# Performance work log

Hardware: AMD Instinct MI355X
Metric: run time of the kernel (lower is better)

## Reference

```python
import jax, jax.numpy as jnp
import numpy as np

TOP_K = 2
SCALE = 1.0  # score_scale_factor

def setup_inputs() -> dict:
    key = jax.random.key(0)
    ks = jax.random.split(key, 8)
    T, D, E, F = 4096, 1024, 8, 4096
    return {
        "hidden_states": jax.random.normal(ks[0], (T, D), jnp.float32),
        "gw1": jax.random.normal(ks[1], (D, D // 4), jnp.float32) * 0.02,
        "gb1": jnp.zeros((D // 4,), jnp.float32),
        "gw2": jax.random.normal(ks[2], (D // 4, D // 16), jnp.float32) * 0.02,
        "gb2": jnp.zeros((D // 16,), jnp.float32),
        "gw3": jax.random.normal(ks[3], (D // 16, E), jnp.float32) * 0.02,
        "w1": jax.random.normal(ks[4], (E, D, F), jnp.float32) * 0.02,
        "b1": jnp.zeros((E, F), jnp.float32),
        "w2": jax.random.normal(ks[5], (E, F, D), jnp.float32) * 0.02,
        "b2": jnp.zeros((E, D), jnp.float32),
    }

def reference(hidden_states, gw1, gb1, gw2, gb2, gw3, w1, b1, w2, b2):
    h = hidden_states                              # [T, D]
    g = jax.nn.relu(h @ gw1 + gb1)
    g = jax.nn.relu(g @ gw2 + gb2)
    router_logits = g @ gw3                        # [T, E]
    probs = jax.nn.softmax(router_logits.astype(jnp.float32), axis=-1)
    top_w, top_i = jax.lax.top_k(probs, TOP_K)     # [T, k]
    top_w = top_w / jnp.sum(top_w, axis=-1, keepdims=True)
    top_w = top_w.astype(h.dtype)
    T, E = router_logits.shape
    # combine weights: scatter normalized top-k weights into dense [T, E]
    cw = jnp.zeros((T, E), h.dtype).at[jnp.arange(T)[:, None], top_i].add(top_w)
    out = jnp.zeros_like(h)
    for e in range(E):  # small fixed expert count
        y = jax.nn.gelu(h @ w1[e] + b1[e]) @ w2[e] + b2[e]
        out = out + y * (cw[:, e:e + 1] * SCALE)
    return out, router_logits
```

## Files before the change

### kernel.cpp

```cpp
#include <hip/hip_runtime.h>
#include <stdint.h>

#define T_  4096
#define D_  1024
#define E_  8
#define F_  4096
#define H1_ 256
#define H2_ 64
#define SCALE_ 1.0f
#define NROW_ (2 * T_)
#define NTILES_ 72

typedef unsigned short ushort_t;
typedef unsigned int   uint32;
typedef __attribute__((ext_vector_type(8))) short  short8;
typedef __attribute__((ext_vector_type(4))) float  f32x4;
typedef __attribute__((ext_vector_type(8))) unsigned short us8;

#define BARRIER() do { asm volatile("" ::: "memory"); __builtin_amdgcn_s_barrier(); asm volatile("" ::: "memory"); } while (0)
#define WAITVM(N) asm volatile("s_waitcnt vmcnt(" #N ")" ::: "memory")

__device__ __forceinline__ ushort_t f2bf(float f) {
  uint32 u = __float_as_uint(f);
  u += 0x7FFFu + ((u >> 16) & 1u);
  return (ushort_t)(u >> 16);
}
__device__ __forceinline__ float gelu_tanh(float x) {
  float u = 0.7978845608028654f * (x + 0.044715f * x * x * x);
  float e = __expf(2.0f * u);
  return 0.5f * x * (1.0f + (1.0f - 2.0f / (e + 1.0f)));
}
__device__ __forceinline__ void gll16(const void* gptr, void* lptr) {
  void* g = const_cast<void*>(gptr);
  __builtin_amdgcn_global_load_lds((__attribute__((address_space(1))) void*)g,
                                   (__attribute__((address_space(3))) void*)lptr,
                                   16, 0, 0);
}

__device__ __forceinline__ void stage4(const ushort_t* a0, const ushort_t* a1,
                                       const ushort_t* b0, const ushort_t* b1,
                                       short8* An, short8* Bn, int w) {
  gll16(a0, An + (w * 2 + 0) * 64);
  gll16(a1, An + (w * 2 + 1) * 64);
  gll16(b0, Bn + (w * 2 + 0) * 64);
  gll16(b1, Bn + (w * 2 + 1) * 64);
}

__device__ __forceinline__ void mfma_step(const short8* Ac, const short8* Bc,
                                          int wr, int wc, int lane, f32x4 acc[4][4]) {
  short8 af[4], bf4[4];
#pragma unroll
  for (int i = 0; i < 4; ++i) af[i] = Ac[(wr * 4 + i) * 64 + lane];
#pragma unroll
  for (int j = 0; j < 4; ++j) bf4[j] = Bc[(wc * 4 + j) * 64 + lane];
#pragma unroll
  for (int i = 0; i < 4; ++i)
#pragma unroll
    for (int j = 0; j < 4; ++j)
      acc[i][j] = __builtin_amdgcn_mfma_f32_16x16x32_bf16(af[i], bf4[j], acc[i][j], 0, 0, 0);
}

__global__ void k_cvt_h(const float* __restrict__ h, ushort_t* __restrict__ hb) {
  int i = (blockIdx.x * 256 + threadIdx.x) * 8;
  float4 a = *(const float4*)(h + i);
  float4 b = *(const float4*)(h + i + 4);
  short8 v;
  v[0] = (short)f2bf(a.x); v[1] = (short)f2bf(a.y);
  v[2] = (short)f2bf(a.z); v[3] = (short)f2bf(a.w);
  v[4] = (short)f2bf(b.x); v[5] = (short)f2bf(b.y);
  v[6] = (short)f2bf(b.z); v[7] = (short)f2bf(b.w);
  *(short8*)(hb + i) = v;
}

__global__ void k_transpose_bf16(const float* __restrict__ in, ushort_t* __restrict__ out,
                                 int R, int C) {
  __shared__ float ltf[64][65];
  const size_t per = (size_t)R * C;
  const float* src = in + per * blockIdx.z;
  ushort_t* dst = out + per * blockIdx.z;
  int r0 = blockIdx.x * 64, c0 = blockIdx.y * 64;
  int tid = threadIdx.x;
  int cg = (tid & 15) * 4;
  int rr = tid >> 4;
#pragma unroll
  for (int rb = 0; rb < 64; rb += 16) {
    int r = rb + rr;
    float4 v = *(const float4*)(src + (size_t)(r0 + r) * C + c0 + cg);
    ltf[r][cg + 0] = v.x; ltf[r][cg + 1] = v.y;
    ltf[r][cg + 2] = v.z; ltf[r][cg + 3] = v.w;
  }
  __syncthreads();
  int c = tid >> 2, rch = (tid & 3) * 16;
  ushort_t tmp[16];
#pragma unroll
  for (int i = 0; i < 16; ++i) tmp[i] = f2bf(ltf[rch + i][c]);
  ushort_t* dp = dst + (size_t)(c0 + c) * R + r0 + rch;
  *(us8*)dp = *(const us8*)&tmp[0];
  *(us8*)(dp + 8) = *(const us8*)&tmp[8];
}

__global__ void k_router1(const float* __restrict__ h, const float* __restrict__ gw1,
                          double* __restrict__ p1) {
  __shared__ float sA[16][65];
  __shared__ float sB[16][65];
  int tx = threadIdx.x, ty = threadIdx.y;
  int tid = ty * 16 + tx;
  int m0 = blockIdx.y * 64, n0 = blockIdx.x * 64;
  int kc = blockIdx.z;
  double acc[4][4] = {};
  for (int k0 = kc * 256; k0 < kc * 256 + 256; k0 += 16) {
    {
      int m = tid & 63, kq = tid >> 6;
      float4 v = *(const float4*)(h + (size_t)(m0 + m) * D_ + k0 + kq * 4);
      sA[kq*4+0][m] = v.x; sA[kq*4+1][m] = v.y; sA[kq*4+2][m] = v.z; sA[kq*4+3][m] = v.w;
    }
    {
      int k = tid >> 4, nq = tid & 15;
      float4 v = *(const float4*)(gw1 + (size_t)(k0 + k) * H1_ + n0 + nq * 4);
      sB[k][nq*4+0] = v.x; sB[k][nq*4+1] = v.y; sB[k][nq*4+2] = v.z; sB[k][nq*4+3] = v.w;
    }
    __syncthreads();
#pragma unroll
    for (int k = 0; k < 16; ++k) {
      float a[4], b[4];
#pragma unroll
      for (int i = 0; i < 4; ++i) a[i] = sA[k][ty + i * 16];
#pragma unroll
      for (int j = 0; j < 4; ++j) b[j] = sB[k][tx * 4 + j];
#pragma unroll
      for (int i = 0; i < 4; ++i)
#pragma unroll
        for (int j = 0; j < 4; ++j)
          acc[i][j] += (double)a[i] * (double)b[j];
    }
    __syncthreads();
  }
  double* pd = p1 + (size_t)kc * T_ * H1_;
  for (int i = 0; i < 4; ++i)
    for (int j = 0; j < 4; ++j) {
      int m = m0 + ty + i * 16, n = n0 + tx * 4 + j;
      pd[(size_t)m * H1_ + n] = acc[i][j];
    }
}

__global__ void k_router23(const double* __restrict__ p1, const float* __restrict__ gb1,
                           const float* __restrict__ gw2, const float* __restrict__ gb2,
                           const float* __restrict__ gw3,
                           float* __restrict__ logits_out, int* __restrict__ tokExp,
                           float* __restrict__ tokW, int* __restrict__ counts) {
  __shared__ double sG1[4][256];
  __shared__ double sG2[4][64];
  __shared__ double sL[4][8];
  int lane = threadIdx.x & 63, wv = threadIdx.x >> 6;
  int t = blockIdx.x * 4 + wv;
  const size_t TH = (size_t)T_ * H1_;
  const double* gp = p1 + (size_t)t * H1_ + lane * 4;
  double s0 = 0, s1 = 0, s2 = 0, s3 = 0;
#pragma unroll
  for (int kc = 0; kc < 4; ++kc) {
    double2 va = *(const double2*)(gp + kc * TH);
    double2 vb = *(const double2*)(gp + kc * TH + 2);
    s0 += va.x; s1 += va.y; s2 += vb.x; s3 += vb.y;
  }
  int hbase = lane * 4;
  s0 += (double)gb1[hbase + 0]; s1 += (double)gb1[hbase + 1];
  s2 += (double)gb1[hbase + 2]; s3 += (double)gb1[hbase + 3];
  sG1[wv][hbase + 0] = s0 > 0.0 ? s0 : 0.0;
  sG1[wv][hbase + 1] = s1 > 0.0 ? s1 : 0.0;
  sG1[wv][hbase + 2] = s2 > 0.0 ? s2 : 0.0;
  sG1[wv][hbase + 3] = s3 > 0.0 ? s3 : 0.0;
  __syncthreads();
  double acc = (double)gb2[lane];
  for (int k = 0; k < H1_; ++k)
    acc += sG1[wv][k] * (double)gw2[k * H2_ + lane];
  sG2[wv][lane] = acc > 0.0 ? acc : 0.0;
  __syncthreads();
  if (lane < 8) {
    double l = 0.0;
    for (int j = 0; j < H2_; ++j) l += sG2[wv][j] * (double)gw3[j * E_ + lane];
    sL[wv][lane] = l;
    logits_out[(size_t)t * E_ + lane] = (float)l;
  }
  __syncthreads();
  if (lane == 0) {
    double best = -1e300, second = -1e300; int bi = 0, si = 0;
    for (int e = 0; e < E_; ++e) {
      double l = sL[wv][e];
      if (l > best)        { second = best; si = bi; best = l; bi = e; }
      else if (l > second) { second = l; si = e; }
    }
    double w0 = 1.0 / (1.0 + exp(second - best));
    tokExp[t*2]   = bi; tokExp[t*2+1] = si;
    tokW[t*2]     = (float)w0;
    tokW[t*2+1]   = (float)(1.0 - w0);
    atomicAdd(&counts[bi], 1);
    atomicAdd(&counts[si], 1);
  }
}

__global__ void k_assign(const int* __restrict__ tokExp, const int* __restrict__ counts,
                         int* cursor, int* __restrict__ list, int* __restrict__ rowOf,
                         int* __restrict__ tileTab) {
  int offs[E_];
  int s = 0;
#pragma unroll
  for (int e = 0; e < E_; ++e) { offs[e] = s; s += counts[e]; }
  if (blockIdx.x == 0 && threadIdx.x == 0) {
    int nt = 0;
    for (int e = 0; e < E_; ++e) {
      int cnt = counts[e];
      for (int m = 0; m * 128 < cnt; ++m) {
        tileTab[nt*3+0] = e;
        tileTab[nt*3+1] = offs[e] + m * 128;
        tileTab[nt*3+2] = (cnt - m * 128) < 128 ? (cnt - m * 128) : 128;
        ++nt;
      }
    }
    for (; nt < NTILES_; ++nt) tileTab[nt*3+0] = -1;
  }
  int t = blockIdx.x * 256 + threadIdx.x;
  for (int k = 0; k < 2; ++k) {
    int e = tokExp[t*2+k];
    int pos = atomicAdd(&cursor[e], 1);
    int row = offs[e] + pos;
    list[row] = t;
    rowOf[t*2+k] = row;
  }
}

__global__ __launch_bounds__(256) void k_moe_ffn1(
    const ushort_t* __restrict__ hb, const ushort_t* __restrict__ w1t,
    const float* __restrict__ b1, ushort_t* __restrict__ act,
    const int* __restrict__ list, const int* __restrict__ tileTab) {
  int ti = blockIdx.y;
  int e = tileTab[ti*3+0];
  if (e < 0) return;
  int rowStart = tileTab[ti*3+1];
  int cntTile  = tileTab[ti*3+2];
  int nBase = blockIdx.x * 128;
  const ushort_t* B = w1t + (size_t)e * F_ * D_;
  int tid = threadIdx.x, w = tid >> 6, lane = tid & 63;
  int m16 = lane & 15, kq = lane >> 4;
  __shared__ short8 lA[2][512];
  __shared__ short8 lB[2][512];
  int gr0 = rowStart + (w * 2) * 16 + m16;
  int gr1 = gr0 + 16;
  int t0 = list[min(gr0, NROW_ - 1)];
  int t1 = list[min(gr1, NROW_ - 1)];
  const ushort_t* aS0 = hb + (size_t)t0 * D_ + kq * 8;
  const ushort_t* aS1 = hb + (size_t)t1 * D_ + kq * 8;
  const ushort_t* bS0 = B + (size_t)(nBase + (w * 2) * 16 + m16) * D_ + kq * 8;
  const ushort_t* bS1 = bS0 + (size_t)16 * D_;
  int wr = w >> 1, wc = w & 1;
  f32x4 acc[4][4] = {};
  short8* Ac = lA[0]; short8* An = lA[1];
  short8* Bc = lB[0]; short8* Bn = lB[1];
  stage4(aS0, aS1, bS0, bS1, Ac, Bc, w);
  const int NSTEP = D_ / 32;
  for (int step = 0; step < NSTEP - 1; ++step) {
    int k0 = (step + 1) * 32;
    stage4(aS0 + k0, aS1 + k0, bS0 + k0, bS1 + k0, An, Bn, w);
    WAITVM(4);
    BARRIER();
    mfma_step(Ac, Bc, wr, wc, lane, acc);
    BARRIER();
    short8* t;
    t = Ac; Ac = An; An = t;
    t = Bc; Bc = Bn; Bn = t;
  }
  WAITVM(0);
  BARRIER();
  mfma_step(Ac, Bc, wr, wc, lane, acc);
  const float* b1e = b1 + (size_t)e * F_;
  int quad = lane >> 4, cn = lane & 15;
#pragma unroll
  for (int i = 0; i < 4; ++i) {
    int lrow = (wr * 4 + i) * 16 + quad * 4;
#pragma unroll
    for (int r = 0; r < 4; ++r) {
      if (lrow + r < cntTile) {
        size_t gr = (size_t)rowStart + lrow + r;
#pragma unroll
        for (int j = 0; j < 4; ++j) {
          int n = nBase + (wc * 4 + j) * 16 + cn;
          float x = acc[i][j][r] + b1e[n];
          act[gr * F_ + n] = f2bf(gelu_tanh(x));
        }
      }
    }
  }
}

__global__ __launch_bounds__(256) void k_moe_ffn2(
    const ushort_t* __restrict__ act, const ushort_t* __restrict__ w2t,
    float* __restrict__ part, const int* __restrict__ tileTab) {
  int ti = blockIdx.y;
  int e = tileTab[ti*3+0];
  if (e < 0) return;
  int rowStart = tileTab[ti*3+1];
  int cntTile  = tileTab[ti*3+2];
  int kc = blockIdx.z;
  int nBase = blockIdx.x * 128;
  const ushort_t* Bw = w2t + (size_t)e * D_ * F_;
  int tid = threadIdx.x, w = tid >> 6, lane = tid & 63;
  int m16 = lane & 15, kq = lane >> 4;
  __shared__ short8 lA[2][512];
  __shared__ short8 lB[2][512];
  int gr0 = rowStart + (w * 2) * 16 + m16;
  int gr1 = gr0 + 16;
  int kBase = kc * (F_ / 2);
  const ushort_t* aS0 = act + (size_t)min(gr0, NROW_ - 1) * F_ + kBase + kq * 8;
  const ushort_t* aS1 = act + (size_t)min(gr1, NROW_ - 1) * F_ + kBase + kq * 8;
  const ushort_t* bS0 = Bw + (size_t)(nBase + (w * 2) * 16 + m16) * F_ + kBase + kq * 8;
  const ushort_t* bS1 = bS0 + (size_t)16 * F_;
  int wr = w >> 1, wc = w & 1;
  f32x4 acc[4][4] = {};
  short8* Ac = lA[0]; short8* An = lA[1];
  short8* Bc = lB[0]; short8* Bn = lB[1];
  stage4(aS0, aS1, bS0, bS1, Ac, Bc, w);
  const int NSTEP = (F_ / 2) / 32;
  for (int step = 0; step < NSTEP - 1; ++step) {
    int k0 = (step + 1) * 32;
    stage4(aS0 + k0, aS1 + k0, bS0 + k0, bS1 + k0, An, Bn, w);
    WAITVM(4);
    BARRIER();
    mfma_step(Ac, Bc, wr, wc, lane, acc);
    BARRIER();
    short8* t;
    t = Ac; Ac = An; An = t;
    t = Bc; Bc = Bn; Bn = t;
  }
  WAITVM(0);
  BARRIER();
  mfma_step(Ac, Bc, wr, wc, lane, acc);
  float* pd = part + (size_t)kc * NROW_ * D_;
  int quad = lane >> 4, cn = lane & 15;
#pragma unroll
  for (int i = 0; i < 4; ++i) {
    int lrow = (wr * 4 + i) * 16 + quad * 4;
#pragma unroll
    for (int r = 0; r < 4; ++r) {
      if (lrow + r < cntTile) {
        size_t gr = (size_t)rowStart + lrow + r;
#pragma unroll
        for (int j = 0; j < 4; ++j) {
          int n = nBase + (wc * 4 + j) * 16 + cn;
          pd[gr * D_ + n] = acc[i][j][r];
        }
      }
    }
  }
}

__global__ void k_combine(const float* __restrict__ part, const int* __restrict__ rowOf,
                          const int* __restrict__ tokExp, const float* __restrict__ tokW,
                          const float* __restrict__ b2, float* __restrict__ out) {
  int t = blockIdx.x;
  int rA = rowOf[t*2], rB = rowOf[t*2+1];
  int eA = tokExp[t*2], eB = tokExp[t*2+1];
  float wA = tokW[t*2] * SCALE_, wB = tokW[t*2+1] * SCALE_;
  int d = threadIdx.x * 4;
  const size_t P = (size_t)NROW_ * D_;
  float4 a0 = *(const float4*)(part + (size_t)rA * D_ + d);
  float4 a1 = *(const float4*)(part + P + (size_t)rA * D_ + d);
  float4 b0 = *(const float4*)(part + (size_t)rB * D_ + d);
  float4 b1 = *(const float4*)(part + P + (size_t)rB * D_ + d);
  float4 ba = *(const float4*)(b2 + (size_t)eA * D_ + d);
  float4 bb = *(const float4*)(b2 + (size_t)eB * D_ + d);
  float4 o;
  o.x = wA * (a0.x + a1.x + ba.x) + wB * (b0.x + b1.x + bb.x);
  o.y = wA * (a0.y + a1.y + ba.y) + wB * (b0.y + b1.y + bb.y);
  o.z = wA * (a0.z + a1.z + ba.z) + wB * (b0.z + b1.z + bb.z);
  o.w = wA * (a0.w + a1.w + ba.w) + wB * (b0.w + b1.w + bb.w);
  *(float4*)(out + (size_t)t * D_ + d) = o;
}

extern "C" void kernel_launch(void* const* d_in, const int* in_sizes, int n_in,
                              void* d_out, int out_size, void* d_ws, size_t ws_size,
                              hipStream_t stream) {
  const float* h   = (const float*)d_in[0];
  const float* gw1 = (const float*)d_in[1];
  const float* gb1 = (const float*)d_in[2];
  const float* gw2 = (const float*)d_in[3];
  const float* gb2 = (const float*)d_in[4];
  const float* gw3 = (const float*)d_in[5];
  const float* w1  = (const float*)d_in[6];
  const float* b1  = (const float*)d_in[7];
  const float* w2  = (const float*)d_in[8];
  const float* b2  = (const float*)d_in[9];
  float* out    = (float*)d_out;
  float* logits = out + (size_t)T_ * D_;

  char* ws = (char*)d_ws;
  size_t o = 0;
  auto alloc = [&](size_t bytes) -> void* {
    o = (o + 255) & ~(size_t)255;
    void* p = ws + o;
    o += bytes;
    return p;
  };
  int*      counts  = (int*)alloc(2 * E_ * 4);
  int*      cursor  = counts + E_;
  int*      tileTab = (int*)alloc((size_t)NTILES_ * 3 * 4);
  int*      tokExp  = (int*)alloc((size_t)T_ * 2 * 4);
  float*    tokW    = (float*)alloc((size_t)T_ * 2 * 4);
  int*      list    = (int*)alloc((size_t)NROW_ * 4);
  int*      rowOf   = (int*)alloc((size_t)NROW_ * 4);
  ushort_t* hb      = (ushort_t*)alloc((size_t)T_ * D_ * 2);
  ushort_t* w2t     = (ushort_t*)alloc((size_t)E_ * D_ * F_ * 2);
  char*     bigA    = (char*)alloc((size_t)NROW_ * F_ * 2);
  double*   p1      = (double*)bigA;
  ushort_t* act     = (ushort_t*)bigA;
  char*     bigB    = (char*)alloc((size_t)E_ * D_ * F_ * 2);
  ushort_t* w1t     = (ushort_t*)bigB;
  float*    part    = (float*)bigB;
  (void)ws_size; (void)in_sizes; (void)n_in; (void)out_size;

  hipMemsetAsync(counts, 0, 2 * E_ * 4, stream);
  k_cvt_h<<<T_ * D_ / 2048, 256, 0, stream>>>(h, hb);
  k_transpose_bf16<<<dim3(D_ / 64, F_ / 64, E_), 256, 0, stream>>>(w1, w1t, D_, F_);
  k_transpose_bf16<<<dim3(F_ / 64, D_ / 64, E_), 256, 0, stream>>>(w2, w2t, F_, D_);
  k_router1<<<dim3(H1_ / 64, T_ / 64, 4), dim3(16, 16), 0, stream>>>(h, gw1, p1);
  k_router23<<<T_ / 4, 256, 0, stream>>>(p1, gb1, gw2, gb2, gw3, logits, tokExp, tokW, counts);
  k_assign<<<T_ / 256, 256, 0, stream>>>(tokExp, counts, cursor, list, rowOf, tileTab);
  k_moe_ffn1<<<dim3(F_ / 128, NTILES_), 256, 0, stream>>>(hb, w1t, b1, act, list, tileTab);
  k_moe_ffn2<<<dim3(D_ / 128, NTILES_, 2), 256, 0, stream>>>(act, w2t, part, tileTab);
  k_combine<<<T_, 256, 0, stream>>>(part, rowOf, tokExp, tokW, b2, out);
}
```

Baseline: 890.2 us.

## Triple-buffer LDS staging in expert FFN GEMMs to drop one barrier per step

```diff
diff --git a/kernel.cpp b/kernel.cpp
--- a/kernel.cpp
+++ b/kernel.cpp
@@ -241,8 +241,8 @@
   const ushort_t* B = w1t + (size_t)e * F_ * D_;
   int tid = threadIdx.x, w = tid >> 6, lane = tid & 63;
   int m16 = lane & 15, kq = lane >> 4;
-  __shared__ short8 lA[2][512];
-  __shared__ short8 lB[2][512];
+  __shared__ short8 lA[3][512];
+  __shared__ short8 lB[3][512];
   int gr0 = rowStart + (w * 2) * 16 + m16;
   int gr1 = gr0 + 16;
   int t0 = list[min(gr0, NROW_ - 1)];
@@ -253,24 +253,23 @@
   const ushort_t* bS1 = bS0 + (size_t)16 * D_;
   int wr = w >> 1, wc = w & 1;
   f32x4 acc[4][4] = {};
-  short8* Ac = lA[0]; short8* An = lA[1];
-  short8* Bc = lB[0]; short8* Bn = lB[1];
-  stage4(aS0, aS1, bS0, bS1, Ac, Bc, w);
+  short8 *A0 = lA[0], *A1 = lA[1], *A2 = lA[2];
+  short8 *B0 = lB[0], *B1 = lB[1], *B2 = lB[2];
+  stage4(aS0, aS1, bS0, bS1, A0, B0, w);
+  stage4(aS0 + 32, aS1 + 32, bS0 + 32, bS1 + 32, A1, B1, w);
   const int NSTEP = D_ / 32;
-  for (int step = 0; step < NSTEP - 1; ++step) {
-    int k0 = (step + 1) * 32;
-    stage4(aS0 + k0, aS1 + k0, bS0 + k0, bS1 + k0, An, Bn, w);
+  for (int t = 0; t < NSTEP - 2; ++t) {
     WAITVM(4);
     BARRIER();
-    mfma_step(Ac, Bc, wr, wc, lane, acc);
-    BARRIER();
-    short8* t;
-    t = Ac; Ac = An; An = t;
-    t = Bc; Bc = Bn; Bn = t;
-  }
-  WAITVM(0);
-  BARRIER();
-  mfma_step(Ac, Bc, wr, wc, lane, acc);
+    int k0 = (t + 2) * 32;
+    stage4(aS0 + k0, aS1 + k0, bS0 + k0, bS1 + k0, A2, B2, w);
+    mfma_step(A0, B0, wr, wc, lane, acc);
+    short8* tp;
+    tp = A0; A0 = A1; A1 = A2; A2 = tp;
+    tp = B0; B0 = B1; B1 = B2; B2 = tp;
+  }
+  WAITVM(4); BARRIER(); mfma_step(A0, B0, wr, wc, lane, acc);
+  WAITVM(0); BARRIER(); mfma_step(A1, B1, wr, wc, lane, acc);
   const float* b1e = b1 + (size_t)e * F_;
   int quad = lane >> 4, cn = lane & 15;
 #pragma unroll
@@ -304,8 +303,8 @@
   const ushort_t* Bw = w2t + (size_t)e * D_ * F_;
   int tid = threadIdx.x, w = tid >> 6, lane = tid & 63;
   int m16 = lane & 15, kq = lane >> 4;
-  __shared__ short8 lA[2][512];
-  __shared__ short8 lB[2][512];
+  __shared__ short8 lA[3][512];
+  __shared__ short8 lB[3][512];
   int gr0 = rowStart + (w * 2) * 16 + m16;
   int gr1 = gr0 + 16;
   int kBase = kc * (F_ / 2);
@@ -315,24 +314,23 @@
   const ushort_t* bS1 = bS0 + (size_t)16 * F_;
   int wr = w >> 1, wc = w & 1;
   f32x4 acc[4][4] = {};
-  short8* Ac = lA[0]; short8* An = lA[1];
-  short8* Bc = lB[0]; short8* Bn = lB[1];
-  stage4(aS0, aS1, bS0, bS1, Ac, Bc, w);
+  short8 *A0 = lA[0], *A1 = lA[1], *A2 = lA[2];
+  short8 *B0 = lB[0], *B1 = lB[1], *B2 = lB[2];
+  stage4(aS0, aS1, bS0, bS1, A0, B0, w);
+  stage4(aS0 + 32, aS1 + 32, bS0 + 32, bS1 + 32, A1, B1, w);
   const int NSTEP = (F_ / 2) / 32;
-  for (int step = 0; step < NSTEP - 1; ++step) {
-    int k0 = (step + 1) * 32;
-    stage4(aS0 + k0, aS1 + k0, bS0 + k0, bS1 + k0, An, Bn, w);
+  for (int t = 0; t < NSTEP - 2; ++t) {
     WAITVM(4);
     BARRIER();
-    mfma_step(Ac, Bc, wr, wc, lane, acc);
-    BARRIER();
-    short8* t;
-    t = Ac; Ac = An; An = t;
-    t = Bc; Bc = Bn; Bn = t;
-  }
-  WAITVM(0);
-  BARRIER();
-  mfma_step(Ac, Bc, wr, wc, lane, acc);
+    int k0 = (t + 2) * 32;
+    stage4(aS0 + k0, aS1 + k0, bS0 + k0, bS1 + k0, A2, B2, w);
+    mfma_step(A0, B0, wr, wc, lane, acc);
+    short8* tp;
+    tp = A0; A0 = A1; A1 = A2; A2 = tp;
+    tp = B0; B0 = B1; B1 = B2; B2 = tp;
+  }
+  WAITVM(4); BARRIER(); mfma_step(A0, B0, wr, wc, lane, acc);
+  WAITVM(0); BARRIER(); mfma_step(A1, B1, wr, wc, lane, acc);
   float* pd = part + (size_t)kc * NROW_ * D_;
   int quad = lane >> 4, cn = lane & 15;
 #pragma unroll
```

Result: slower. 938.3 us (+5.4%).

## Enlarge MoE GEMM tiles to 256x256 with 512-thread blocks

Applied to the files above, without the earlier changes.

```diff
diff --git a/kernel.cpp b/kernel.cpp
--- a/kernel.cpp
+++ b/kernel.cpp
@@ -9,7 +9,7 @@
 #define H2_ 64
 #define SCALE_ 1.0f
 #define NROW_ (2 * T_)
-#define NTILES_ 72
+#define NT2_ 40
 
 typedef unsigned short ushort_t;
 typedef unsigned int   uint32;
@@ -46,15 +46,15 @@
   gll16(b1, Bn + (w * 2 + 1) * 64);
 }
 
-__device__ __forceinline__ void mfma_step(const short8* Ac, const short8* Bc,
-                                          int wr, int wc, int lane, f32x4 acc[4][4]) {
-  short8 af[4], bf4[4];
-#pragma unroll
-  for (int i = 0; i < 4; ++i) af[i] = Ac[(wr * 4 + i) * 64 + lane];
+__device__ __forceinline__ void mfma_step256(const short8* Ac, const short8* Bc,
+                                             int wr, int wc, int lane, f32x4 acc[8][4]) {
+  short8 af[8], bf4[4];
+#pragma unroll
+  for (int i = 0; i < 8; ++i) af[i] = Ac[(wr * 8 + i) * 64 + lane];
 #pragma unroll
   for (int j = 0; j < 4; ++j) bf4[j] = Bc[(wc * 4 + j) * 64 + lane];
 #pragma unroll
-  for (int i = 0; i < 4; ++i)
+  for (int i = 0; i < 8; ++i)
 #pragma unroll
     for (int j = 0; j < 4; ++j)
       acc[i][j] = __builtin_amdgcn_mfma_f32_16x16x32_bf16(af[i], bf4[j], acc[i][j], 0, 0, 0);
@@ -209,14 +209,14 @@
     int nt = 0;
     for (int e = 0; e < E_; ++e) {
       int cnt = counts[e];
-      for (int m = 0; m * 128 < cnt; ++m) {
+      for (int m = 0; m * 256 < cnt; ++m) {
         tileTab[nt*3+0] = e;
-        tileTab[nt*3+1] = offs[e] + m * 128;
-        tileTab[nt*3+2] = (cnt - m * 128) < 128 ? (cnt - m * 128) : 128;
+        tileTab[nt*3+1] = offs[e] + m * 256;
+        tileTab[nt*3+2] = (cnt - m * 256) < 256 ? (cnt - m * 256) : 256;
         ++nt;
       }
     }
-    for (; nt < NTILES_; ++nt) tileTab[nt*3+0] = -1;
+    for (; nt < NT2_; ++nt) tileTab[nt*3+0] = -1;
   }
   int t = blockIdx.x * 256 + threadIdx.x;
   for (int k = 0; k < 2; ++k) {
@@ -228,7 +228,7 @@
   }
 }
 
-__global__ __launch_bounds__(256) void k_moe_ffn1(
+__global__ __launch_bounds__(512, 2) void k_moe_ffn1(
     const ushort_t* __restrict__ hb, const ushort_t* __restrict__ w1t,
     const float* __restrict__ b1, ushort_t* __restrict__ act,
     const int* __restrict__ list, const int* __restrict__ tileTab) {
@@ -237,53 +237,51 @@
   if (e < 0) return;
   int rowStart = tileTab[ti*3+1];
   int cntTile  = tileTab[ti*3+2];
-  int nBase = blockIdx.x * 128;
+  int nBase = blockIdx.x * 256;
   const ushort_t* B = w1t + (size_t)e * F_ * D_;
   int tid = threadIdx.x, w = tid >> 6, lane = tid & 63;
   int m16 = lane & 15, kq = lane >> 4;
-  __shared__ short8 lA[2][512];
-  __shared__ short8 lB[2][512];
-  int gr0 = rowStart + (w * 2) * 16 + m16;
+  __shared__ short8 lA[2][1024];
+  __shared__ short8 lB[2][1024];
+  int gr0 = rowStart + w * 32 + m16;
   int gr1 = gr0 + 16;
   int t0 = list[min(gr0, NROW_ - 1)];
   int t1 = list[min(gr1, NROW_ - 1)];
   const ushort_t* aS0 = hb + (size_t)t0 * D_ + kq * 8;
   const ushort_t* aS1 = hb + (size_t)t1 * D_ + kq * 8;
-  const ushort_t* bS0 = B + (size_t)(nBase + (w * 2) * 16 + m16) * D_ + kq * 8;
+  const ushort_t* bS0 = B + (size_t)(nBase + w * 32 + m16) * D_ + kq * 8;
   const ushort_t* bS1 = bS0 + (size_t)16 * D_;
-  int wr = w >> 1, wc = w & 1;
-  f32x4 acc[4][4] = {};
-  short8* Ac = lA[0]; short8* An = lA[1];
-  short8* Bc = lB[0]; short8* Bn = lB[1];
-  stage4(aS0, aS1, bS0, bS1, Ac, Bc, w);
+  int wr = w >> 2, wc = w & 3;
+  f32x4 acc[8][4] = {};
+  stage4(aS0, aS1, bS0, bS1, lA[0], lB[0], w);
   const int NSTEP = D_ / 32;
-  for (int step = 0; step < NSTEP - 1; ++step) {
-    int k0 = (step + 1) * 32;
-    stage4(aS0 + k0, aS1 + k0, bS0 + k0, bS1 + k0, An, Bn, w);
+  for (int t = 0; t < NSTEP - 1; ++t) {
+    int k0 = (t + 1) * 32;
+    stage4(aS0 + k0, aS1 + k0, bS0 + k0, bS1 + k0, lA[(t + 1) & 1], lB[(t + 1) & 1], w);
     WAITVM(4);
     BARRIER();
-    mfma_step(Ac, Bc, wr, wc, lane, acc);
+    mfma_step256(lA[t & 1], lB[t & 1], wr, wc, lane, acc);
     BARRIER();
-    short8* t;
-    t = Ac; Ac = An; An = t;
-    t = Bc; Bc = Bn; Bn = t;
   }
   WAITVM(0);
   BARRIER();
-  mfma_step(Ac, Bc, wr, wc, lane, acc);
+  mfma_step256(lA[(NSTEP - 1) & 1], lB[(NSTEP - 1) & 1], wr, wc, lane, acc);
   const float* b1e = b1 + (size_t)e * F_;
   int quad = lane >> 4, cn = lane & 15;
-#pragma unroll
-  for (int i = 0; i < 4; ++i) {
-    int lrow = (wr * 4 + i) * 16 + quad * 4;
+  float bj[4];
+#pragma unroll
+  for (int j = 0; j < 4; ++j) bj[j] = b1e[nBase + wc * 64 + j * 16 + cn];
+#pragma unroll
+  for (int i = 0; i < 8; ++i) {
+    int lrow = wr * 128 + i * 16 + quad * 4;
 #pragma unroll
     for (int r = 0; r < 4; ++r) {
       if (lrow + r < cntTile) {
         size_t gr = (size_t)rowStart + lrow + r;
 #pragma unroll
         for (int j = 0; j < 4; ++j) {
-          int n = nBase + (wc * 4 + j) * 16 + cn;
-          float x = acc[i][j][r] + b1e[n];
+          int n = nBase + wc * 64 + j * 16 + cn;
+          float x = acc[i][j][r] + bj[j];
           act[gr * F_ + n] = f2bf(gelu_tanh(x));
         }
       }
@@ -291,7 +289,7 @@
   }
 }
 
-__global__ __launch_bounds__(256) void k_moe_ffn2(
+__global__ __launch_bounds__(512, 2) void k_moe_ffn2(
     const ushort_t* __restrict__ act, const ushort_t* __restrict__ w2t,
     float* __restrict__ part, const int* __restrict__ tileTab) {
   int ti = blockIdx.y;
@@ -300,51 +298,46 @@
   int rowStart = tileTab[ti*3+1];
   int cntTile  = tileTab[ti*3+2];
   int kc = blockIdx.z;
-  int nBase = blockIdx.x * 128;
+  int nBase = blockIdx.x * 256;
   const ushort_t* Bw = w2t + (size_t)e * D_ * F_;
   int tid = threadIdx.x, w = tid >> 6, lane = tid & 63;
   int m16 = lane & 15, kq = lane >> 4;
-  __shared__ short8 lA[2][512];
-  __shared__ short8 lB[2][512];
-  int gr0 = rowStart + (w * 2) * 16 + m16;
+  __shared__ short8 lA[2][1024];
+  __shared__ short8 lB[2][1024];
+  int gr0 = rowStart + w * 32 + m16;
   int gr1 = gr0 + 16;
   int kBase = kc * (F_ / 2);
   const ushort_t* aS0 = act + (size_t)min(gr0, NROW_ - 1) * F_ + kBase + kq * 8;
   const ushort_t* aS1 = act + (size_t)min(gr1, NROW_ - 1) * F_ + kBase + kq * 8;
-  const ushort_t* bS0 = Bw + (size_t)(nBase + (w * 2) * 16 + m16) * F_ + kBase + kq * 8;
+  const ushort_t* bS0 = Bw + (size_t)(nBase + w * 32 + m16) * F_ + kBase + kq * 8;
   const ushort_t* bS1 = bS0 + (size_t)16 * F_;
-  int wr = w >> 1, wc = w & 1;
-  f32x4 acc[4][4] = {};
-  short8* Ac = lA[0]; short8* An = lA[1];
-  short8* Bc = lB[0]; short8* Bn = lB[1];
-  stage4(aS0, aS1, bS0, bS1, Ac, Bc, w);
+  int wr = w >> 2, wc = w & 3;
+  f32x4 acc[8][4] = {};
+  stage4(aS0, aS1, bS0, bS1, lA[0], lB[0], w);
   const int NSTEP = (F_ / 2) / 32;
-  for (int step = 0; step < NSTEP - 1; ++step) {
-    int k0 = (step + 1) * 32;
-    stage4(aS0 + k0, aS1 + k0, bS0 + k0, bS1 + k0, An, Bn, w);
+  for (int t = 0; t < NSTEP - 1; ++t) {
+    int k0 = (t + 1) * 32;
+    stage4(aS0 + k0, aS1 + k0, bS0 + k0, bS1 + k0, lA[(t + 1) & 1], lB[(t + 1) & 1], w);
     WAITVM(4);
     BARRIER();
-    mfma_step(Ac, Bc, wr, wc, lane, acc);
+    mfma_step256(lA[t & 1], lB[t & 1], wr, wc, lane, acc);
     BARRIER();
-    short8* t;
-    t = Ac; Ac = An; An = t;
-    t = Bc; Bc = Bn; Bn = t;
   }
   WAITVM(0);
   BARRIER();
-  mfma_step(Ac, Bc, wr, wc, lane, acc);
+  mfma_step256(lA[(NSTEP - 1) & 1], lB[(NSTEP - 1) & 1], wr, wc, lane, acc);
   float* pd = part + (size_t)kc * NROW_ * D_;
   int quad = lane >> 4, cn = lane & 15;
 #pragma unroll
-  for (int i = 0; i < 4; ++i) {
-    int lrow = (wr * 4 + i) * 16 + quad * 4;
+  for (int i = 0; i < 8; ++i) {
+    int lrow = wr * 128 + i * 16 + quad * 4;
 #pragma unroll
     for (int r = 0; r < 4; ++r) {
       if (lrow + r < cntTile) {
         size_t gr = (size_t)rowStart + lrow + r;
 #pragma unroll
         for (int j = 0; j < 4; ++j) {
-          int n = nBase + (wc * 4 + j) * 16 + cn;
+          int n = nBase + wc * 64 + j * 16 + cn;
           pd[gr * D_ + n] = acc[i][j][r];
         }
       }
@@ -401,7 +394,7 @@
   };
   int*      counts  = (int*)alloc(2 * E_ * 4);
   int*      cursor  = counts + E_;
-  int*      tileTab = (int*)alloc((size_t)NTILES_ * 3 * 4);
+  int*      tileTab = (int*)alloc((size_t)NT2_ * 3 * 4);
   int*      tokExp  = (int*)alloc((size_t)T_ * 2 * 4);
   float*    tokW    = (float*)alloc((size_t)T_ * 2 * 4);
   int*      list    = (int*)alloc((size_t)NROW_ * 4);
@@ -423,7 +416,7 @@
   k_router1<<<dim3(H1_ / 64, T_ / 64, 4), dim3(16, 16), 0, stream>>>(h, gw1, p1);
   k_router23<<<T_ / 4, 256, 0, stream>>>(p1, gb1, gw2, gb2, gw3, logits, tokExp, tokW, counts);
   k_assign<<<T_ / 256, 256, 0, stream>>>(tokExp, counts, cursor, list, rowOf, tileTab);
-  k_moe_ffn1<<<dim3(F_ / 128, NTILES_), 256, 0, stream>>>(hb, w1t, b1, act, list, tileTab);
-  k_moe_ffn2<<<dim3(D_ / 128, NTILES_, 2), 256, 0, stream>>>(act, w2t, part, tileTab);
+  k_moe_ffn1<<<dim3(F_ / 256, NT2_), 512, 0, stream>>>(hb, w1t, b1, act, list, tileTab);
+  k_moe_ffn2<<<dim3(D_ / 256, NT2_, 2), 512, 0, stream>>>(act, w2t, part, tileTab);
   k_combine<<<T_, 256, 0, stream>>>(part, rowOf, tokExp, tokW, b2, out);
 }
```

Result: slower. 936.2 us (+5.2%).
